# Performance work log

Hardware: AMD Instinct MI355X
Metric: run time of the kernel (lower is better)

The kernel has to match this reference:

```python
import jax, jax.numpy as jnp
import numpy as np

N = 100000
NEG_SLOPE = 0.2
ALPHA = 0.5


def _glorot(key, shape):
    fan_in, fan_out = shape[0], shape[-1]
    lim = jnp.sqrt(6.0 / (fan_in + fan_out))
    return jax.random.uniform(key, shape, jnp.float32, -lim, lim)


def setup_inputs() -> dict:
    key = jax.random.key(0)
    ks = jax.random.split(key, 16)
    x = jax.random.normal(ks[0], (N, 512), jnp.float32)
    spatial_edge_index = jax.random.randint(ks[1], (2, 800000), 0, N, jnp.int64)
    gene_sim_edge_index = jax.random.randint(ks[2], (2, 800000), 0, N, jnp.int64)
    # spatial GAT params (in=512 -> hid=256)
    W_sp = _glorot(ks[3], (512, 256)); a_src_sp = _glorot(ks[4], (256,)); a_dst_sp = _glorot(ks[5], (256,)); b_sp = jnp.zeros((256,), jnp.float32)
    # gene-sim GAT params
    W_gs = _glorot(ks[6], (512, 256)); a_src_gs = _glorot(ks[7], (256,)); a_dst_gs = _glorot(ks[8], (256,)); b_gs = jnp.zeros((256,), jnp.float32)
    # fusion GAT params (hid=256 -> out=64)
    W_fu = _glorot(ks[9], (256, 64)); a_src_fu = _glorot(ks[10], (64,)); a_dst_fu = _glorot(ks[11], (64,)); b_fu = jnp.zeros((64,), jnp.float32)
    return {"x": x, "spatial_edge_index": spatial_edge_index, "gene_sim_edge_index": gene_sim_edge_index,
            "W_sp": W_sp, "a_src_sp": a_src_sp, "a_dst_sp": a_dst_sp, "b_sp": b_sp,
            "W_gs": W_gs, "a_src_gs": a_src_gs, "a_dst_gs": a_dst_gs, "b_gs": b_gs,
            "W_fu": W_fu, "a_src_fu": a_src_fu, "a_dst_fu": a_dst_fu, "b_fu": b_fu}


def gat_conv(x, edge_index, W, a_src, a_dst, bias):
    """PyG GATConv, heads=1, concat=False, add_self_loops=True."""
    n = x.shape[0]
    h = x @ W  # [N, H]
    loops = jnp.arange(n, dtype=edge_index.dtype)
    src = jnp.concatenate([edge_index[0], loops])  # message source j
    dst = jnp.concatenate([edge_index[1], loops])  # aggregation target i
    e = jax.nn.leaky_relu((h @ a_src)[src] + (h @ a_dst)[dst], NEG_SLOPE)  # [E+N]
    # segment softmax over incoming edges of each dst node
    m = jax.ops.segment_max(e, dst, num_segments=n)
    ex = jnp.exp(e - m[dst])
    denom = jax.ops.segment_sum(ex, dst, num_segments=n)
    coef = ex / denom[dst]
    out = jax.ops.segment_sum(coef[:, None] * h[src], dst, num_segments=n)
    return out + bias


def reference(x, spatial_edge_index, gene_sim_edge_index,
              W_sp, a_src_sp, a_dst_sp, b_sp,
              W_gs, a_src_gs, a_dst_gs, b_gs,
              W_fu, a_src_fu, a_dst_fu, b_fu):
    h_spatial = jax.nn.elu(gat_conv(x, spatial_edge_index, W_sp, a_src_sp, a_dst_sp, b_sp))
    h_gene = jax.nn.elu(gat_conv(x, gene_sim_edge_index, W_gs, a_src_gs, a_dst_gs, b_gs))
    h_fused = ALPHA * h_gene + (1.0 - ALPHA) * h_spatial
    return gat_conv(h_fused, spatial_edge_index, W_fu, a_src_fu, a_dst_fu, b_fu)
```

## Files before the change

kernel.cpp:

```cpp
#include <hip/hip_runtime.h>
#include <math.h>


#define NEG_SLOPE 0.2f

typedef __attribute__((ext_vector_type(8))) short bf16x8;
typedef __attribute__((ext_vector_type(4))) float f32x4;

__device__ __forceinline__ unsigned short f2bf(float f) {
  unsigned int u = __float_as_uint(f);
  u = (u + 0x7FFFu + ((u >> 16) & 1u)) >> 16;
  return (unsigned short)u;
}
__device__ __forceinline__ float bf2f(unsigned short u) {
  return __uint_as_float((unsigned int)u << 16);
}
__device__ __forceinline__ int rl_i(int v, int l) {
  return __builtin_amdgcn_readlane(v, l);
}
__device__ __forceinline__ float rl_f(float v, int l) {
  return __uint_as_float(__builtin_amdgcn_readlane(__float_as_uint(v), l));
}

#define GLOAD16(g, l)                                                   \
  __builtin_amdgcn_global_load_lds(                                     \
      (const __attribute__((address_space(1))) void*)(g),               \
      (__attribute__((address_space(3))) void*)(l), 16, 0, 0)

__global__ __launch_bounds__(256) void wt_bf16_all(const float* __restrict__ W_sp,
                                                   const float* __restrict__ W_gs,
                                                   const float* __restrict__ W_fu,
                                                   unsigned short* __restrict__ wt_sp,
                                                   unsigned short* __restrict__ wt_gs,
                                                   unsigned short* __restrict__ wt_fu) {
  const int i = blockIdx.x * 256 + threadIdx.x;
  if (i < 131072) {
    const int k = i >> 8, n = i & 255;
    wt_sp[n * 512 + k] = f2bf(W_sp[i]);
  } else if (i < 262144) {
    const int j = i - 131072;
    const int k = j >> 8, n = j & 255;
    wt_gs[n * 512 + k] = f2bf(W_gs[j]);
  } else if (i < 278528) {
    const int j = i - 262144;
    const int k = j >> 6, n = j & 63;
    wt_fu[n * 256 + k] = f2bf(W_fu[j]);
  }
}

__global__ __launch_bounds__(256) void hist2(const int* __restrict__ dst_sp,
                                             const int* __restrict__ dst_gs,
                                             int* __restrict__ deg_sp,
                                             int* __restrict__ deg_gs,
                                             int* __restrict__ ord_sp,
                                             int* __restrict__ ord_gs, int E) {
  const int m = blockIdx.x * 256 + threadIdx.x;
  if (m < E) {
    ord_sp[m] = atomicAdd(&deg_sp[dst_sp[m]], 1);
    ord_gs[m] = atomicAdd(&deg_gs[dst_gs[m]], 1);
  }
}

__global__ __launch_bounds__(256) void scan1_2(const int* __restrict__ deg_sp,
                                               const int* __restrict__ deg_gs,
                                               int* __restrict__ rs_sp,
                                               int* __restrict__ rs_gs,
                                               int* __restrict__ parts2, int N) {
  __shared__ int sm[256];
  const int* deg = blockIdx.y ? deg_gs : deg_sp;
  int* rs = blockIdx.y ? rs_gs : rs_sp;
  int* parts = parts2 + blockIdx.y * 512;
  const int i = blockIdx.x * 256 + threadIdx.x;
  const int v = (i < N) ? deg[i] : 0;
  sm[threadIdx.x] = v;
  __syncthreads();
  for (int off = 1; off < 256; off <<= 1) {
    const int x = (threadIdx.x >= off) ? sm[threadIdx.x - off] : 0;
    __syncthreads();
    sm[threadIdx.x] += x;
    __syncthreads();
  }
  if (i < N) rs[i] = sm[threadIdx.x] - v;
  if (threadIdx.x == 255) parts[blockIdx.x] = sm[255];
}

__global__ __launch_bounds__(512) void scan2_2(int* __restrict__ parts2, int nb) {
  __shared__ int sm[512];
  int* parts = parts2 + blockIdx.x * 512;
  const int t = threadIdx.x;
  const int v = (t < nb) ? parts[t] : 0;
  sm[t] = v;
  __syncthreads();
  for (int off = 1; off < 512; off <<= 1) {
    const int x = (t >= off) ? sm[t - off] : 0;
    __syncthreads();
    sm[t] += x;
    __syncthreads();
  }
  if (t < nb) parts[t] = sm[t] - v;
}

__global__ __launch_bounds__(256) void scan3_2(int* __restrict__ rs_sp,
                                               int* __restrict__ rs_gs,
                                               const int* __restrict__ parts2,
                                               int N, int E) {
  int* rs = blockIdx.y ? rs_gs : rs_sp;
  const int* parts = parts2 + blockIdx.y * 512;
  const int i = blockIdx.x * 256 + threadIdx.x;
  if (i < N) rs[i] += parts[blockIdx.x];
  if (i == 0) rs[N] = E;
}

__global__ __launch_bounds__(256) void scatter2(const int* __restrict__ ei_sp,
                                                const int* __restrict__ ei_gs,
                                                const int* __restrict__ rs_sp,
                                                const int* __restrict__ rs_gs,
                                                const int* __restrict__ ord_sp,
                                                const int* __restrict__ ord_gs,
                                                int* __restrict__ csr_sp,
                                                int* __restrict__ csr_gs, int E) {
  const int m = blockIdx.x * 256 + threadIdx.x;
  if (m >= E) return;
  csr_sp[rs_sp[ei_sp[E + m]] + ord_sp[m]] = ei_sp[m];
  csr_gs[rs_gs[ei_gs[E + m]] + ord_gs[m]] = ei_gs[m];
}

__global__ __launch_bounds__(1024) void gemm2_fused(const float* __restrict__ x,
                                                    const unsigned short* __restrict__ wsp,
                                                    const unsigned short* __restrict__ wgs,
                                                    unsigned short* __restrict__ hb_sp,
                                                    unsigned short* __restrict__ hb_gs,
                                                    int M) {
  __shared__ unsigned short sA[128 * 64];
  __shared__ unsigned short sW[2][256 * 64];
  const int tid = threadIdx.x;
  const int w = tid >> 6, l = tid & 63;
  const int whalf = w >> 3;
  const int wsub = w & 7;
  const int wr = wsub >> 2;
  const int wq = wsub & 3;
  const int bm = blockIdx.x * 128;

  const int arow0 = tid >> 4;
  const int acol4 = (tid & 15) * 4;
  int g0 = bm + arow0;       g0 = g0 < M ? g0 : M - 1;
  int g1 = bm + arow0 + 64;  g1 = g1 < M ? g1 : M - 1;
  const float* __restrict__ ap0 = x + (size_t)g0 * 512 + acol4;
  const float* __restrict__ ap1 = x + (size_t)g1 * 512 + acol4;
  const int abyte0 = (arow0 * 128 + acol4 * 2) ^ ((arow0 & 7) << 4);
  const int abyte1 = ((arow0 + 64) * 128 + acol4 * 2) ^ (((arow0 + 64) & 7) << 4);

  const unsigned short* __restrict__ wtp = whalf ? wgs : wsp;
  const int wrow_in_ch = l >> 3;
  const int wbyte = ((l & 7) * 16) ^ ((wrow_in_ch & 7) << 4);

  f32x4 acc[4][4] = {};
  for (int k0 = 0; k0 < 512; k0 += 64) {
    __syncthreads();
    {
      const float4 v0 = *(const float4*)(ap0 + k0);
      const float4 v1 = *(const float4*)(ap1 + k0);
      ushort4 o0, o1;
      o0.x = f2bf(v0.x); o0.y = f2bf(v0.y); o0.z = f2bf(v0.z); o0.w = f2bf(v0.w);
      o1.x = f2bf(v1.x); o1.y = f2bf(v1.y); o1.z = f2bf(v1.z); o1.w = f2bf(v1.w);
      *(ushort4*)(((char*)sA) + abyte0) = o0;
      *(ushort4*)(((char*)sA) + abyte1) = o1;
    }
#pragma unroll
    for (int c = 0; c < 4; ++c) {
      const int ch = c * 8 + wsub;
      const int grow = ch * 8 + wrow_in_ch;
      const char* g = (const char*)wtp + (size_t)grow * 1024 + (size_t)k0 * 2 + wbyte;
      GLOAD16(g, ((char*)sW[whalf]) + ch * 1024);
    }
    __syncthreads();
#pragma unroll
    for (int ks = 0; ks < 2; ++ks) {
      const int cb = ks * 64 + (l >> 4) * 16;
      bf16x8 af[4], bf[4];
#pragma unroll
      for (int m = 0; m < 4; ++m) {
        const int r = wr * 64 + m * 16 + (l & 15);
        af[m] = *(const bf16x8*)(((const char*)sA) + r * 128 + (cb ^ ((r & 7) << 4)));
      }
#pragma unroll
      for (int n = 0; n < 4; ++n) {
        const int r = wq * 64 + n * 16 + (l & 15);
        bf[n] = *(const bf16x8*)(((const char*)sW[whalf]) + r * 128 + (cb ^ ((r & 7) << 4)));
      }
#pragma unroll
      for (int m = 0; m < 4; ++m)
#pragma unroll
        for (int n = 0; n < 4; ++n)
          acc[m][n] = __builtin_amdgcn_mfma_f32_16x16x32_bf16(af[m], bf[n], acc[m][n], 0, 0, 0);
    }
  }
  unsigned short* __restrict__ outp = whalf ? hb_gs : hb_sp;
#pragma unroll
  for (int m = 0; m < 4; ++m) {
#pragma unroll
    for (int r = 0; r < 4; ++r) {
      const int row = bm + wr * 64 + m * 16 + (l >> 4) * 4 + r;
      if (row < M) {
#pragma unroll
        for (int n = 0; n < 4; ++n)
          outp[(size_t)row * 256 + wq * 64 + n * 16 + (l & 15)] = f2bf(acc[m][n][r]);
      }
    }
  }
}

template <int BN>
__global__ __launch_bounds__(256) void gemm_bf16_nt(const unsigned short* __restrict__ A,
                                                    const unsigned short* __restrict__ Bt,
                                                    unsigned short* __restrict__ C,
                                                    int M, int Nc, int K) {
  constexpr int BM = 128, BK = 64;
  constexpr int NW = BN / 64;
  constexpr int MW = 4 / NW;
  constexpr int MF = (BM / MW) / 16;
  constexpr int NF = 4;
  constexpr int ACW = (BM * BK * 2 / 1024) / 4;
  constexpr int BCW = (BN * BK * 2 / 1024) / 4;
  __shared__ unsigned short sA[BM * BK];
  __shared__ unsigned short sB[BN * BK];
  const int tid = threadIdx.x;
  const int w = tid >> 6, l = tid & 63;
  const int wr = w / NW, wc = w % NW;
  const int bm = blockIdx.x * BM;
  const int bn = blockIdx.y * BN;
  const int crow = l >> 3;
  const int cbyte = (l & 7) * 16;

  f32x4 acc[MF][NF] = {};
  for (int k0 = 0; k0 < K; k0 += BK) {
    __syncthreads();
#pragma unroll
    for (int c = 0; c < ACW; ++c) {
      const int ch = w * ACW + c;
      int row = bm + ch * 8 + crow;
      row = row < M ? row : M - 1;
      const char* g = (const char*)A + (size_t)row * K * 2 + (size_t)k0 * 2 + cbyte;
      GLOAD16(g, ((char*)sA) + ch * 1024);
    }
#pragma unroll
    for (int c = 0; c < BCW; ++c) {
      const int ch = w * BCW + c;
      const int row = bn + ch * 8 + crow;
      const char* g = (const char*)Bt + (size_t)row * K * 2 + (size_t)k0 * 2 + cbyte;
      GLOAD16(g, ((char*)sB) + ch * 1024);
    }
    __syncthreads();
#pragma unroll
    for (int ks = 0; ks < 2; ++ks) {
      bf16x8 af[MF], bfr[NF];
#pragma unroll
      for (int m = 0; m < MF; ++m) {
        const int r = wr * (BM / MW) + m * 16 + (l & 15);
        af[m] = *(const bf16x8*)&sA[r * BK + ks * 32 + (l >> 4) * 8];
      }
#pragma unroll
      for (int n = 0; n < NF; ++n) {
        const int r = wc * 64 + n * 16 + (l & 15);
        bfr[n] = *(const bf16x8*)&sB[r * BK + ks * 32 + (l >> 4) * 8];
      }
#pragma unroll
      for (int m = 0; m < MF; ++m)
#pragma unroll
        for (int n = 0; n < NF; ++n)
          acc[m][n] = __builtin_amdgcn_mfma_f32_16x16x32_bf16(af[m], bfr[n], acc[m][n], 0, 0, 0);
    }
  }
#pragma unroll
  for (int m = 0; m < MF; ++m) {
#pragma unroll
    for (int r = 0; r < 4; ++r) {
      const int row = bm + wr * (BM / MW) + m * 16 + (l >> 4) * 4 + r;
      if (row < M) {
#pragma unroll
        for (int n = 0; n < NF; ++n)
          C[(size_t)row * Nc + bn + wc * 64 + n * 16 + (l & 15)] = f2bf(acc[m][n][r]);
      }
    }
  }
}

__global__ __launch_bounds__(256) void alpha2_256(const ushort4* __restrict__ hsp,
                                                  const ushort4* __restrict__ hgs,
                                                  const float* __restrict__ av_sp_s,
                                                  const float* __restrict__ av_sp_d,
                                                  const float* __restrict__ av_gs_s,
                                                  const float* __restrict__ av_gs_d,
                                                  float* __restrict__ asrc_sp,
                                                  float* __restrict__ adst_sp,
                                                  float* __restrict__ asrc_gs,
                                                  float* __restrict__ adst_gs, int N) {
  const int wave = (int)((blockIdx.x * (size_t)blockDim.x + threadIdx.x) >> 6);
  const int lane = threadIdx.x & 63;
  if (wave >= N) return;
  const ushort4 h1 = hsp[(size_t)wave * 64 + lane];
  const ushort4 h2 = hgs[(size_t)wave * 64 + lane];
  const float4 s1 = ((const float4*)av_sp_s)[lane];
  const float4 d1 = ((const float4*)av_sp_d)[lane];
  const float4 s2 = ((const float4*)av_gs_s)[lane];
  const float4 d2 = ((const float4*)av_gs_d)[lane];
  const float a0 = bf2f(h1.x), a1 = bf2f(h1.y), a2 = bf2f(h1.z), a3 = bf2f(h1.w);
  const float b0 = bf2f(h2.x), b1 = bf2f(h2.y), b2 = bf2f(h2.z), b3 = bf2f(h2.w);
  float p0 = a0 * s1.x + a1 * s1.y + a2 * s1.z + a3 * s1.w;
  float p1 = a0 * d1.x + a1 * d1.y + a2 * d1.z + a3 * d1.w;
  float p2 = b0 * s2.x + b1 * s2.y + b2 * s2.z + b3 * s2.w;
  float p3 = b0 * d2.x + b1 * d2.y + b2 * d2.z + b3 * d2.w;
#pragma unroll
  for (int off = 32; off; off >>= 1) {
    p0 += __shfl_down(p0, off);
    p1 += __shfl_down(p1, off);
    p2 += __shfl_down(p2, off);
    p3 += __shfl_down(p3, off);
  }
  if (lane == 0) {
    asrc_sp[wave] = p0; adst_sp[wave] = p1;
    asrc_gs[wave] = p2; adst_gs[wave] = p3;
  }
}

__global__ __launch_bounds__(256) void alpha64(const unsigned short* __restrict__ h,
                                               const float* __restrict__ a_src,
                                               const float* __restrict__ a_dst,
                                               float* __restrict__ asrc,
                                               float* __restrict__ adst, int N) {
  const int wave = (int)((blockIdx.x * (size_t)blockDim.x + threadIdx.x) >> 6);
  const int lane = threadIdx.x & 63;
  if (wave >= N) return;
  const float hv = bf2f(h[(size_t)wave * 64 + lane]);
  float ps = hv * a_src[lane];
  float pd = hv * a_dst[lane];
#pragma unroll
  for (int off = 32; off; off >>= 1) {
    ps += __shfl_down(ps, off);
    pd += __shfl_down(pd, off);
  }
  if (lane == 0) { asrc[wave] = ps; adst[wave] = pd; }
}

template <int EPI>
__global__ __launch_bounds__(256) void agg_csr256(const int* __restrict__ rs,
                                                  const int* __restrict__ csr,
                                                  const float* __restrict__ asrc,
                                                  const float* __restrict__ adst,
                                                  const ushort4* __restrict__ h4,
                                                  const float* __restrict__ bias,
                                                  const ushort4* __restrict__ other16,
                                                  ushort4* __restrict__ out16, int N) {
  const int d = (int)((blockIdx.x * (size_t)blockDim.x + threadIdx.x) >> 6);
  const int lane = threadIdx.x & 63;
  if (d >= N) return;
  const float ad = adst[d];

  float e = asrc[d] + ad;
  e = e > 0.f ? e : NEG_SLOPE * e;
  const float wself = expf(e);
  float denl = (lane == 0) ? wself : 0.f;
  const ushort4 hv = h4[(size_t)d * 64 + lane];
  float ax = wself * bf2f(hv.x), ay = wself * bf2f(hv.y),
        az = wself * bf2f(hv.z), aw = wself * bf2f(hv.w);

  const int base = rs[d], mend = rs[d + 1];
  for (int c = base; c < mend; c += 64) {
    const int m = c + lane;
    int s = 0;
    float w = 0.f;
    if (m < mend) {
      s = csr[m];
      float e2 = asrc[s] + ad;
      e2 = e2 > 0.f ? e2 : NEG_SLOPE * e2;
      w = expf(e2);
    }
    denl += w;
    const int cnt = min(64, mend - c);
    int j = 0;
    for (; j + 3 < cnt; j += 4) {
      const int s0 = rl_i(s, j), s1 = rl_i(s, j + 1), s2 = rl_i(s, j + 2), s3 = rl_i(s, j + 3);
      const float w0 = rl_f(w, j), w1 = rl_f(w, j + 1), w2 = rl_f(w, j + 2), w3 = rl_f(w, j + 3);
      const ushort4 a0 = h4[(size_t)s0 * 64 + lane];
      const ushort4 a1 = h4[(size_t)s1 * 64 + lane];
      const ushort4 a2 = h4[(size_t)s2 * 64 + lane];
      const ushort4 a3 = h4[(size_t)s3 * 64 + lane];
      ax += w0 * bf2f(a0.x) + w1 * bf2f(a1.x) + w2 * bf2f(a2.x) + w3 * bf2f(a3.x);
      ay += w0 * bf2f(a0.y) + w1 * bf2f(a1.y) + w2 * bf2f(a2.y) + w3 * bf2f(a3.y);
      az += w0 * bf2f(a0.z) + w1 * bf2f(a1.z) + w2 * bf2f(a2.z) + w3 * bf2f(a3.z);
      aw += w0 * bf2f(a0.w) + w1 * bf2f(a1.w) + w2 * bf2f(a2.w) + w3 * bf2f(a3.w);
    }
    for (; j < cnt; ++j) {
      const int sj = rl_i(s, j);
      const float wj = rl_f(w, j);
      const ushort4 aj = h4[(size_t)sj * 64 + lane];
      ax += wj * bf2f(aj.x);
      ay += wj * bf2f(aj.y);
      az += wj * bf2f(aj.z);
      aw += wj * bf2f(aj.w);
    }
  }
#pragma unroll
  for (int off = 32; off; off >>= 1) denl += __shfl_xor(denl, off);
  const float inv = 1.f / denl;

  const float4 b4 = ((const float4*)bias)[lane];
  float v[4] = {ax * inv + b4.x, ay * inv + b4.y, az * inv + b4.z, aw * inv + b4.w};
#pragma unroll
  for (int j = 0; j < 4; ++j) v[j] = v[j] > 0.f ? v[j] : (expf(v[j]) - 1.f);
  ushort4 pk;
  if (EPI == 2) {
    const ushort4 ov = other16[(size_t)d * 64 + lane];
    pk.x = f2bf(0.5f * v[0] + 0.5f * bf2f(ov.x));
    pk.y = f2bf(0.5f * v[1] + 0.5f * bf2f(ov.y));
    pk.z = f2bf(0.5f * v[2] + 0.5f * bf2f(ov.z));
    pk.w = f2bf(0.5f * v[3] + 0.5f * bf2f(ov.w));
  } else {
    pk.x = f2bf(v[0]); pk.y = f2bf(v[1]); pk.z = f2bf(v[2]); pk.w = f2bf(v[3]);
  }
  out16[(size_t)d * 64 + lane] = pk;
}

__global__ __launch_bounds__(256) void agg_csr64(const int* __restrict__ rs,
                                                 const int* __restrict__ csr,
                                                 const float* __restrict__ asrc,
                                                 const float* __restrict__ adst,
                                                 const unsigned short* __restrict__ h,
                                                 const float* __restrict__ bias,
                                                 float* __restrict__ outb, int N) {
  const int d = (int)((blockIdx.x * (size_t)blockDim.x + threadIdx.x) >> 6);
  const int lane = threadIdx.x & 63;
  if (d >= N) return;
  const float ad = adst[d];

  float e = asrc[d] + ad;
  e = e > 0.f ? e : NEG_SLOPE * e;
  const float wself = expf(e);
  float denl = (lane == 0) ? wself : 0.f;
  float acc = wself * bf2f(h[(size_t)d * 64 + lane]);

  const int base = rs[d], mend = rs[d + 1];
  for (int c = base; c < mend; c += 64) {
    const int m = c + lane;
    int s = 0;
    float w = 0.f;
    if (m < mend) {
      s = csr[m];
      float e2 = asrc[s] + ad;
      e2 = e2 > 0.f ? e2 : NEG_SLOPE * e2;
      w = expf(e2);
    }
    denl += w;
    const int cnt = min(64, mend - c);
    int j = 0;
    for (; j + 3 < cnt; j += 4) {
      const int s0 = rl_i(s, j), s1 = rl_i(s, j + 1), s2 = rl_i(s, j + 2), s3 = rl_i(s, j + 3);
      const float w0 = rl_f(w, j), w1 = rl_f(w, j + 1), w2 = rl_f(w, j + 2), w3 = rl_f(w, j + 3);
      const float a0 = bf2f(h[(size_t)s0 * 64 + lane]);
      const float a1 = bf2f(h[(size_t)s1 * 64 + lane]);
      const float a2 = bf2f(h[(size_t)s2 * 64 + lane]);
      const float a3 = bf2f(h[(size_t)s3 * 64 + lane]);
      acc += w0 * a0 + w1 * a1 + w2 * a2 + w3 * a3;
    }
    for (; j < cnt; ++j) {
      const int sj = rl_i(s, j);
      const float wj = rl_f(w, j);
      acc += wj * bf2f(h[(size_t)sj * 64 + lane]);
    }
  }
#pragma unroll
  for (int off = 32; off; off >>= 1) denl += __shfl_xor(denl, off);
  outb[(size_t)d * 64 + lane] = acc / denl + bias[lane];
}

extern "C" void kernel_launch(void* const* d_in, const int* in_sizes, int n_in,
                              void* d_out, int out_size, void* d_ws, size_t ws_size,
                              hipStream_t stream) {
  const float* x        = (const float*)d_in[0];
  const int*   ei_sp    = (const int*)d_in[1];
  const int*   ei_gs    = (const int*)d_in[2];
  const float* W_sp     = (const float*)d_in[3];
  const float* a_src_sp = (const float*)d_in[4];
  const float* a_dst_sp = (const float*)d_in[5];
  const float* b_sp     = (const float*)d_in[6];
  const float* W_gs     = (const float*)d_in[7];
  const float* a_src_gs = (const float*)d_in[8];
  const float* a_dst_gs = (const float*)d_in[9];
  const float* b_gs     = (const float*)d_in[10];
  const float* W_fu     = (const float*)d_in[11];
  const float* a_src_fu = (const float*)d_in[12];
  const float* a_dst_fu = (const float*)d_in[13];
  const float* b_fu     = (const float*)d_in[14];
  float* out = (float*)d_out;

  const int N = in_sizes[0] / 512;
  const int E = in_sizes[1] / 2;
  const int nb = (N + 255) / 256;

  unsigned short* wt_sp = (unsigned short*)d_ws;
  unsigned short* wt_gs = wt_sp + 256 * 512;
  unsigned short* wt_fu = wt_gs + 256 * 512;
  unsigned short* hb_sp = wt_fu + 64 * 256;
  unsigned short* hb_gs = hb_sp + (size_t)N * 256;
  unsigned short* B3    = hb_gs + (size_t)N * 256;
  unsigned short* hfb   = B3 + (size_t)N * 256;
  float* asrc_sp = (float*)(hfb + (size_t)N * 256);
  float* adst_sp = asrc_sp + N;
  float* asrc_gs = adst_sp + N;
  float* adst_gs = asrc_gs + N;
  int* rs_sp  = (int*)(adst_gs + N);
  int* rs_gs  = rs_sp + (N + 1);
  int* csr_sp = rs_gs + (N + 1);
  int* csr_gs = csr_sp + E;
  int* deg_sp = csr_gs + E;
  int* deg_gs = deg_sp + N;
  int* parts2 = deg_gs + N;
  int* ord_sp = parts2 + 1024;
  int* ord_gs = ord_sp + E;

  unsigned short* hfu = B3;

  const int BLK = 256;
  const int eGrid = (E + BLK - 1) / BLK;
  const int nodeWaveGrid = (N + 3) / 4;
  const dim3 gFu((N + 127) / 128, 1);

  hipMemsetAsync(deg_sp, 0, (size_t)2 * N * 4, stream);
  hist2<<<eGrid, BLK, 0, stream>>>(ei_sp + E, ei_gs + E, deg_sp, deg_gs,
                                   ord_sp, ord_gs, E);
  scan1_2<<<dim3(nb, 2), BLK, 0, stream>>>(deg_sp, deg_gs, rs_sp, rs_gs, parts2, N);
  scan2_2<<<2, 512, 0, stream>>>(parts2, nb);
  scan3_2<<<dim3(nb, 2), BLK, 0, stream>>>(rs_sp, rs_gs, parts2, N, E);
  scatter2<<<eGrid, BLK, 0, stream>>>(ei_sp, ei_gs, rs_sp, rs_gs, ord_sp, ord_gs,
                                      csr_sp, csr_gs, E);

  wt_bf16_all<<<(278528 + 255) / 256, BLK, 0, stream>>>(W_sp, W_gs, W_fu,
                                                        wt_sp, wt_gs, wt_fu);

  gemm2_fused<<<(N + 127) / 128, 1024, 0, stream>>>(x, wt_sp, wt_gs, hb_sp, hb_gs, N);

  alpha2_256<<<nodeWaveGrid, BLK, 0, stream>>>((const ushort4*)hb_sp,
                                               (const ushort4*)hb_gs,
                                               a_src_sp, a_dst_sp, a_src_gs, a_dst_gs,
                                               asrc_sp, adst_sp, asrc_gs, adst_gs, N);

  agg_csr256<1><<<nodeWaveGrid, BLK, 0, stream>>>(rs_sp, csr_sp, asrc_sp, adst_sp,
                                                  (const ushort4*)hb_sp, b_sp,
                                                  nullptr, (ushort4*)B3, N);

  agg_csr256<2><<<nodeWaveGrid, BLK, 0, stream>>>(rs_gs, csr_gs, asrc_gs, adst_gs,
                                                  (const ushort4*)hb_gs, b_gs,
                                                  (const ushort4*)B3, (ushort4*)hfb, N);

  gemm_bf16_nt<64><<<gFu, BLK, 0, stream>>>(hfb, wt_fu, hfu, N, 64, 256);
  alpha64<<<nodeWaveGrid, BLK, 0, stream>>>(hfu, a_src_fu, a_dst_fu,
                                            asrc_sp, adst_sp, N);
  agg_csr64<<<nodeWaveGrid, BLK, 0, stream>>>(rs_sp, csr_sp, asrc_sp, adst_sp,
                                              hfu, b_fu, out, N);
}
```

Measured before the change: 491.7 us.

## Double-buffer weight tiles and prefetch x rows in the fused dual GEMM

The fused spatial/gene GEMM now uses two LDS buffers for the weight tiles. The next k-slice of W is loaded into the spare buffer, and the next x rows are fetched into registers while the MFMAs for the current slice run. This removes the leading barrier from each iteration and hides global load latency behind compute. The cost is double the weight LDS footprint, which brings total shared memory to about 144KB per block and relies on the larger LDS of gfx950. It also adds extra register pressure from the prefetched floats.

```diff
diff --git a/kernel.cpp b/kernel.cpp
--- a/kernel.cpp
+++ b/kernel.cpp
@@ -132,7 +132,7 @@
                                                     unsigned short* __restrict__ hb_gs,
                                                     int M) {
   __shared__ unsigned short sA[128 * 64];
-  __shared__ unsigned short sW[2][256 * 64];
+  __shared__ unsigned short sW[2][2][256 * 64];
   const int tid = threadIdx.x;
   const int w = tid >> 6, l = tid & 63;
   const int whalf = w >> 3;
@@ -154,26 +154,43 @@
   const int wrow_in_ch = l >> 3;
   const int wbyte = ((l & 7) * 16) ^ ((wrow_in_ch & 7) << 4);
 
+#define STAGE_W(BUF, K0)                                                          \
+  _Pragma("unroll")                                                               \
+  for (int c = 0; c < 4; ++c) {                                                   \
+    const int ch = c * 8 + wsub;                                                  \
+    const int grow = ch * 8 + wrow_in_ch;                                         \
+    const char* g = (const char*)wtp + (size_t)grow * 1024 + (size_t)(K0)*2 + wbyte; \
+    GLOAD16(g, ((char*)sW[BUF][whalf]) + ch * 1024);                              \
+  }
+
+#define WRITE_SA(V0, V1)                                                          \
+  {                                                                               \
+    ushort4 o0, o1;                                                               \
+    o0.x = f2bf((V0).x); o0.y = f2bf((V0).y); o0.z = f2bf((V0).z); o0.w = f2bf((V0).w); \
+    o1.x = f2bf((V1).x); o1.y = f2bf((V1).y); o1.z = f2bf((V1).z); o1.w = f2bf((V1).w); \
+    *(ushort4*)(((char*)sA) + abyte0) = o0;                                       \
+    *(ushort4*)(((char*)sA) + abyte1) = o1;                                       \
+  }
+
   f32x4 acc[4][4] = {};
+  {
+    const float4 v0 = *(const float4*)ap0;
+    const float4 v1 = *(const float4*)ap1;
+    STAGE_W(0, 0)
+    WRITE_SA(v0, v1)
+  }
+  __syncthreads();
+
+  int buf = 0;
   for (int k0 = 0; k0 < 512; k0 += 64) {
-    __syncthreads();
-    {
-      const float4 v0 = *(const float4*)(ap0 + k0);
-      const float4 v1 = *(const float4*)(ap1 + k0);
-      ushort4 o0, o1;
-      o0.x = f2bf(v0.x); o0.y = f2bf(v0.y); o0.z = f2bf(v0.z); o0.w = f2bf(v0.w);
-      o1.x = f2bf(v1.x); o1.y = f2bf(v1.y); o1.z = f2bf(v1.z); o1.w = f2bf(v1.w);
-      *(ushort4*)(((char*)sA) + abyte0) = o0;
-      *(ushort4*)(((char*)sA) + abyte1) = o1;
-    }
-#pragma unroll
-    for (int c = 0; c < 4; ++c) {
-      const int ch = c * 8 + wsub;
-      const int grow = ch * 8 + wrow_in_ch;
-      const char* g = (const char*)wtp + (size_t)grow * 1024 + (size_t)k0 * 2 + wbyte;
-      GLOAD16(g, ((char*)sW[whalf]) + ch * 1024);
-    }
-    __syncthreads();
+    const bool pf = (k0 < 448);
+    float4 v0, v1;
+    if (pf) {
+      STAGE_W(buf ^ 1, k0 + 64)
+      v0 = *(const float4*)(ap0 + k0 + 64);
+      v1 = *(const float4*)(ap1 + k0 + 64);
+    }
+    const unsigned short* __restrict__ sWc = sW[buf][whalf];
 #pragma unroll
     for (int ks = 0; ks < 2; ++ks) {
       const int cb = ks * 64 + (l >> 4) * 16;
@@ -186,7 +203,7 @@
 #pragma unroll
       for (int n = 0; n < 4; ++n) {
         const int r = wq * 64 + n * 16 + (l & 15);
-        bf[n] = *(const bf16x8*)(((const char*)sW[whalf]) + r * 128 + (cb ^ ((r & 7) << 4)));
+        bf[n] = *(const bf16x8*)(((const char*)sWc) + r * 128 + (cb ^ ((r & 7) << 4)));
       }
 #pragma unroll
       for (int m = 0; m < 4; ++m)
@@ -194,7 +211,17 @@
         for (int n = 0; n < 4; ++n)
           acc[m][n] = __builtin_amdgcn_mfma_f32_16x16x32_bf16(af[m], bf[n], acc[m][n], 0, 0, 0);
     }
-  }
+    if (pf) {
+      __builtin_amdgcn_s_barrier();
+      asm volatile("" ::: "memory");
+      WRITE_SA(v0, v1)
+      __syncthreads();
+      buf ^= 1;
+    }
+  }
+#undef STAGE_W
+#undef WRITE_SA
+
   unsigned short* __restrict__ outp = whalf ? hb_gs : hb_sp;
 #pragma unroll
   for (int m = 0; m < 4; ++m) {
```

Result: no change. 494.0 us (+0.5%).
